# Kernel tuning notes

Measured on AMD Instinct MI355X. Metric: run time of the kernel, lower is better.

The kernel has to match this reference:

```python
import jax, jax.numpy as jnp
import numpy as np

ENC_H = 128
DEC_H = 256
DEC_STEPS = 10


def _gru_cell(x, h, Wih, Whh, bih, bhh):
    # PyTorch GRU cell, gate order (r, z, n)
    gi = x @ Wih.T + bih          # (B, 3H)
    gh = h @ Whh.T + bhh          # (B, 3H)
    H = h.shape[-1]
    ir, iz, inn = gi[:, :H], gi[:, H:2 * H], gi[:, 2 * H:]
    hr, hz, hn = gh[:, :H], gh[:, H:2 * H], gh[:, 2 * H:]
    r = jax.nn.sigmoid(ir + hr)
    z = jax.nn.sigmoid(iz + hz)
    n = jnp.tanh(inn + r * hn)
    return (1.0 - z) * n + z * h


def setup_inputs() -> dict:
    key = jax.random.key(0)
    ks = jax.random.split(key, 12)
    B, S = 4096, 128
    s = 0.1
    return {
        "x": jax.random.normal(ks[0], (B, S, 5), jnp.float32),
        "y": jax.random.normal(ks[1], (B, S, 1), jnp.float32),
        "enc_Wih": jax.random.normal(ks[2], (3 * ENC_H, 5), jnp.float32) * s,
        "enc_Whh": jax.random.normal(ks[3], (3 * ENC_H, ENC_H), jnp.float32) * s,
        "enc_bih": jax.random.normal(ks[4], (3 * ENC_H,), jnp.float32) * s,
        "enc_bhh": jax.random.normal(ks[5], (3 * ENC_H,), jnp.float32) * s,
        "dec_Wih": jax.random.normal(ks[6], (3 * DEC_H, ENC_H + 1), jnp.float32) * s,
        "dec_Whh": jax.random.normal(ks[7], (3 * DEC_H, DEC_H), jnp.float32) * s,
        "dec_bih": jax.random.normal(ks[8], (3 * DEC_H,), jnp.float32) * s,
        "dec_bhh": jax.random.normal(ks[9], (3 * DEC_H,), jnp.float32) * s,
        "lin_W": jax.random.normal(ks[10], (4, DEC_H), jnp.float32) * s,
        "lin_b": jax.random.normal(ks[11], (4,), jnp.float32) * s,
    }


def reference(x, y, enc_Wih, enc_Whh, enc_bih, enc_bhh,
              dec_Wih, dec_Whh, dec_bih, dec_bhh, lin_W, lin_b):
    B, S, _ = x.shape
    xs = jnp.transpose(x, (1, 0, 2))   # (S, B, 5)
    ys = jnp.transpose(y, (1, 0, 2))   # (S, B, 1)

    # Encoder: only the final hidden state (contex) is consumed downstream.
    h0 = jnp.zeros((B, ENC_H), x.dtype)

    def enc_step(h, xt):
        return _gru_cell(xt, h, enc_Wih, enc_Whh, enc_bih, enc_bhh), None

    contex, _ = jax.lax.scan(enc_step, h0, xs)   # (B, 128)

    # Decoder: initial hidden is ones (torch.ones_like(shape)), 10 steps.
    hdec0 = jnp.ones((B, DEC_H), x.dtype)

    def dec_step(h, yt):
        xt = jnp.concatenate([contex, yt], axis=-1)   # (B, 129)
        h2 = _gru_cell(xt, h, dec_Wih, dec_Whh, dec_bih, dec_bhh)
        out = h2 @ lin_W.T + lin_b                    # (B, 4)
        return h2, out

    _, outs = jax.lax.scan(dec_step, hdec0, ys[:DEC_STEPS])  # (10, B, 4)

    # res starts as ones; only first 10 rows written.
    res = jnp.ones((S, B, 4), x.dtype).at[:DEC_STEPS].set(outs)
    return jnp.transpose(res, (1, 0, 2))   # (B, S, 4)
```

## Files before the change

### kernel.cpp

```cpp
#include <hip/hip_runtime.h>

#define B_SZ 4096
#define S_SZ 128
#define XD 5
#define EH 128
#define DH 256
#define DSTEPS 10

typedef short v8s __attribute__((ext_vector_type(8)));
typedef float v4f __attribute__((ext_vector_type(4)));

__device__ __forceinline__ float bf2f(unsigned short u) {
    union { unsigned int i; float f; } v; v.i = ((unsigned int)u) << 16; return v.f;
}
__device__ __forceinline__ unsigned short f2bf(float f) {
    union { float f; unsigned int i; } v; v.f = f;
    unsigned int x = v.i;
    return (unsigned short)((x + 0x7FFFu + ((x >> 16) & 1u)) >> 16);
}
__device__ __forceinline__ float fexp2(float x) { return __builtin_amdgcn_exp2f(x); }
__device__ __forceinline__ float frcp(float x) { return __builtin_amdgcn_rcpf(x); }
__device__ __forceinline__ float sigmoidf_(float x) {
    return frcp(1.f + fexp2(-1.44269504088896f * x));
}
__device__ __forceinline__ float tanhf_(float x) {
    float e = fexp2(2.88539008177793f * x);
    return 1.f - 2.f * frcp(e + 1.f);
}

__global__ __launch_bounds__(512) void enc_kernel(
    const float* __restrict__ x,
    const float* __restrict__ Wih32,
    const float* __restrict__ Whh32,
    const float* __restrict__ bih,
    const float* __restrict__ bhh,
    const float* __restrict__ dWih,
    const float* __restrict__ dWhh,
    unsigned short* __restrict__ wihp,
    unsigned short* __restrict__ dWhh_bf,
    unsigned short* __restrict__ ctex)
{
    __shared__ unsigned short xs[S_SZ][16][8];
    __shared__ unsigned short hb[2][16][136];
    __shared__ unsigned short zpad[8];

    const int tid = threadIdx.x;
    const int bid = blockIdx.x;
    const int wv = tid >> 6;
    const int lane = tid & 63;
    const int n = lane & 15;
    const int kg = lane >> 4;
    const int r0 = bid * 16;

    for (int i = bid * 512 + tid; i < 768 * 256; i += 131072)
        dWhh_bf[i] = f2bf(dWhh[i]);
    for (int i = bid * 512 + tid; i < 768 * 136; i += 131072) {
        int col = i / 136, k = i - col * 136;
        wihp[i] = (k < 129) ? f2bf(dWih[col * 129 + k]) : (unsigned short)0;
    }

    for (int i = tid; i < 2 * 16 * 136; i += 512) ((unsigned short*)hb)[i] = 0;
    if (tid < 8) zpad[tid] = 0;
    for (int i = tid; i < 16 * S_SZ * 8; i += 512) {
        int m = i >> 10;
        int rem = i & 1023;
        int t = rem >> 3;
        int j = rem & 7;
        unsigned short v = 0;
        if (j < XD) v = f2bf(x[(size_t)(r0 + m) * (S_SZ * XD) + t * XD + j]);
        xs[t][m][j] = v;
    }

    const int colw = wv * 16 + n;
    v8s fw[3][4];
    v8s fx[3];
    #pragma unroll
    for (int g = 0; g < 3; ++g) {
        int gcol = g * EH + colw;
        #pragma unroll
        for (int kt = 0; kt < 4; ++kt) {
            const float* p = &Whh32[(size_t)gcol * EH + kt * 32 + kg * 8];
            float4 lo = *(const float4*)p;
            float4 hi = *(const float4*)(p + 4);
            v8s f;
            f[0] = (short)f2bf(lo.x); f[1] = (short)f2bf(lo.y);
            f[2] = (short)f2bf(lo.z); f[3] = (short)f2bf(lo.w);
            f[4] = (short)f2bf(hi.x); f[5] = (short)f2bf(hi.y);
            f[6] = (short)f2bf(hi.z); f[7] = (short)f2bf(hi.w);
            fw[g][kt] = f;
        }
        v8s t = {0, 0, 0, 0, 0, 0, 0, 0};
        if (kg == 0) {
            const float* p = &Wih32[gcol * XD];
            #pragma unroll
            for (int j = 0; j < XD; ++j) t[j] = (short)f2bf(p[j]);
        }
        fx[g] = t;
    }
    const float b_r  = bih[colw]          + bhh[colw];
    const float b_z  = bih[EH + colw]     + bhh[EH + colw];
    const float bi_n = bih[2 * EH + colw];
    const float bh_n = bhh[2 * EH + colw];

    float hst[4] = {0.f, 0.f, 0.f, 0.f};
    __syncthreads();

    #pragma unroll 2
    for (int t = 0; t < S_SZ; ++t) {
        const int p = t & 1;
        v8s a[4];
        #pragma unroll
        for (int kt = 0; kt < 4; ++kt)
            a[kt] = *(const v8s*)&hb[p][n][kt * 32 + kg * 8];
        const unsigned short* xsrc = (kg == 0) ? &xs[t][n][0] : &zpad[0];
        v8s ax = *(const v8s*)xsrc;

        v4f accr  = {b_r, b_r, b_r, b_r};
        v4f accz  = {b_z, b_z, b_z, b_z};
        v4f acchn = {bh_n, bh_n, bh_n, bh_n};
        v4f accin = {bi_n, bi_n, bi_n, bi_n};
        #pragma unroll
        for (int kt = 0; kt < 4; ++kt) {
            accr  = __builtin_amdgcn_mfma_f32_16x16x32_bf16(a[kt], fw[0][kt], accr, 0, 0, 0);
            accz  = __builtin_amdgcn_mfma_f32_16x16x32_bf16(a[kt], fw[1][kt], accz, 0, 0, 0);
            acchn = __builtin_amdgcn_mfma_f32_16x16x32_bf16(a[kt], fw[2][kt], acchn, 0, 0, 0);
        }
        accr  = __builtin_amdgcn_mfma_f32_16x16x32_bf16(ax, fx[0], accr, 0, 0, 0);
        accz  = __builtin_amdgcn_mfma_f32_16x16x32_bf16(ax, fx[1], accz, 0, 0, 0);
        accin = __builtin_amdgcn_mfma_f32_16x16x32_bf16(ax, fx[2], accin, 0, 0, 0);

        #pragma unroll
        for (int e = 0; e < 4; ++e) {
            float r = sigmoidf_(accr[e]);
            float z = sigmoidf_(accz[e]);
            float nn = tanhf_(accin[e] + r * acchn[e]);
            float h = (1.f - z) * nn + z * hst[e];
            hst[e] = h;
            hb[1 - p][kg * 4 + e][colw] = f2bf(h);
        }
        __syncthreads();
    }
    #pragma unroll
    for (int e = 0; e < 4; ++e)
        ctex[(size_t)(r0 + kg * 4 + e) * EH + colw] = f2bf(hst[e]);
}

__global__ __launch_bounds__(1024)
__attribute__((amdgpu_waves_per_eu(4, 4)))
void dec_all_kernel(
    const unsigned short* __restrict__ dWhh_bf,
    const unsigned short* __restrict__ wihp,
    const float* __restrict__ dbih,
    const float* __restrict__ dbhh,
    const float* __restrict__ y,
    const unsigned short* __restrict__ ctex,
    const float* __restrict__ linW,
    const float* __restrict__ linb,
    float* __restrict__ out)
{
    __shared__ unsigned short hshf[32 * 16 * 8];
    __shared__ unsigned short wshnf[32 * 256 * 8];
    __shared__ unsigned short lwf[32 * 16 * 8];

    const int tid = threadIdx.x;
    const int w = tid >> 6;
    const int lane = tid & 63;
    const int n = lane & 15;
    const int kg = lane >> 4;
    const int rb = blockIdx.x * 16;
    const int hcol = w * 16 + n;

    for (int i = tid; i < 8192; i += 1024) {
        int wcol = i >> 5, kc = i & 31;
        uint4 v = *(const uint4*)&dWhh_bf[(size_t)(512 + wcol) * 256 + kc * 8];
        *(uint4*)&wshnf[(kc * 256 + wcol) * 8] = v;
    }
    if (tid < 512) {
        int col = tid >> 5, kc = tid & 31;
        unsigned short v8[8];
        #pragma unroll
        for (int j = 0; j < 8; ++j)
            v8[j] = (col < 4) ? f2bf(linW[col * 256 + kc * 8 + j]) : (unsigned short)0;
        *(uint4*)&lwf[(kc * 16 + col) * 8] = *(uint4*)v8;
    }
    for (int i = tid; i < 32 * 16 * 8; i += 1024) hshf[i] = 0x3F80;

    v8s fB[2][8];
    #pragma unroll
    for (int g = 0; g < 2; ++g)
        #pragma unroll
        for (int kt = 0; kt < 8; ++kt)
            fB[g][kt] = *(const v8s*)&dWhh_bf[(size_t)(g * 256 + hcol) * 256 + kt * 32 + kg * 8];

    const float bR0 = dbih[hcol] + dbhh[hcol];
    const float bZ0 = dbih[DH + hcol] + dbhh[DH + hcol];
    const float bN0 = dbih[2 * DH + hcol];
    const float bN  = dbhh[2 * DH + hcol];
    const float wy0 = bf2f(wihp[(size_t)(0 * DH + hcol) * 136 + 128]);
    const float wy1 = bf2f(wihp[(size_t)(1 * DH + hcol) * 136 + 128]);
    const float wy2 = bf2f(wihp[(size_t)(2 * DH + hcol) * 136 + 128]);

    v4f gvr = {bR0, bR0, bR0, bR0};
    v4f gvz = {bZ0, bZ0, bZ0, bZ0};
    v4f gvn = {bN0, bN0, bN0, bN0};
    #pragma unroll
    for (int kt = 0; kt < 4; ++kt) {
        v8s a  = *(const v8s*)&ctex[(size_t)(rb + n) * EH + kt * 32 + kg * 8];
        v8s b0 = *(const v8s*)&wihp[(size_t)(0 * DH + hcol) * 136 + kt * 32 + kg * 8];
        v8s b1 = *(const v8s*)&wihp[(size_t)(1 * DH + hcol) * 136 + kt * 32 + kg * 8];
        v8s b2 = *(const v8s*)&wihp[(size_t)(2 * DH + hcol) * 136 + kt * 32 + kg * 8];
        gvr = __builtin_amdgcn_mfma_f32_16x16x32_bf16(a, b0, gvr, 0, 0, 0);
        gvz = __builtin_amdgcn_mfma_f32_16x16x32_bf16(a, b1, gvz, 0, 0, 0);
        gvn = __builtin_amdgcn_mfma_f32_16x16x32_bf16(a, b2, gvn, 0, 0, 0);
    }

    const float lb = linb[n & 3];
    const int wfrag = ((w >> 1) * 4 + ((2 * w + (n >> 3)) & 3)) * 128 + (n & 7);

    float hprev[4] = {1.f, 1.f, 1.f, 1.f};
    __syncthreads();

    for (int t = 0; t < DSTEPS; ++t) {
        float yv[4];
        #pragma unroll
        for (int e = 0; e < 4; ++e)
            yv[e] = y[(size_t)(rb + kg * 4 + e) * S_SZ + t];

        v4f accr = {0.f, 0.f, 0.f, 0.f};
        v4f accz = {0.f, 0.f, 0.f, 0.f};
        v4f accn = {bN, bN, bN, bN};
        #pragma unroll
        for (int kt = 0; kt < 8; ++kt) {
            v8s a   = *(const v8s*)&hshf[((kt * 4 + kg) * 16 + n) * 8];
            v8s bn_ = *(const v8s*)&wshnf[((kt * 4 + kg) * 256 + hcol) * 8];
            accr = __builtin_amdgcn_mfma_f32_16x16x32_bf16(a, fB[0][kt], accr, 0, 0, 0);
            accz = __builtin_amdgcn_mfma_f32_16x16x32_bf16(a, fB[1][kt], accz, 0, 0, 0);
            accn = __builtin_amdgcn_mfma_f32_16x16x32_bf16(a, bn_,      accn, 0, 0, 0);
        }
        __syncthreads();

        #pragma unroll
        for (int e = 0; e < 4; ++e) {
            float r  = sigmoidf_(gvr[e] + yv[e] * wy0 + accr[e]);
            float z  = sigmoidf_(gvz[e] + yv[e] * wy1 + accz[e]);
            float nn = tanhf_(gvn[e] + yv[e] * wy2 + r * accn[e]);
            float h  = nn + z * (hprev[e] - nn);
            hprev[e] = h;
            hshf[wfrag + (kg * 4 + e) * 8] = f2bf(h);
        }
        __syncthreads();

        if (w == 0) {
            v4f o4 = {0.f, 0.f, 0.f, 0.f};
            #pragma unroll
            for (int kt = 0; kt < 8; ++kt) {
                v8s a = *(const v8s*)&hshf[((kt * 4 + kg) * 16 + n) * 8];
                v8s b = *(const v8s*)&lwf[((kt * 4 + kg) * 16 + n) * 8];
                o4 = __builtin_amdgcn_mfma_f32_16x16x32_bf16(a, b, o4, 0, 0, 0);
            }
            if (n < 4) {
                #pragma unroll
                for (int e = 0; e < 4; ++e)
                    out[(size_t)(rb + kg * 4 + e) * (S_SZ * 4) + t * 4 + n] = o4[e] + lb;
            }
        }
    }

    for (int j = tid; j < 16 * 512; j += 1024) {
        int row = j >> 9, c = j & 511;
        if (c >= DSTEPS * 4) out[(size_t)(rb + row) * 512 + c] = 1.0f;
    }
}

extern "C" void kernel_launch(void* const* d_in, const int* in_sizes, int n_in,
                              void* d_out, int out_size, void* d_ws, size_t ws_size,
                              hipStream_t stream)
{
    const float* x    = (const float*)d_in[0];
    const float* y    = (const float*)d_in[1];
    const float* eWih = (const float*)d_in[2];
    const float* eWhh = (const float*)d_in[3];
    const float* ebih = (const float*)d_in[4];
    const float* ebhh = (const float*)d_in[5];
    const float* dWih = (const float*)d_in[6];
    const float* dWhh = (const float*)d_in[7];
    const float* dbih = (const float*)d_in[8];
    const float* dbhh = (const float*)d_in[9];
    const float* linW = (const float*)d_in[10];
    const float* linb = (const float*)d_in[11];
    float* out = (float*)d_out;

    char* ws = (char*)d_ws;
    unsigned short* wihp    = (unsigned short*)(ws);
    unsigned short* dWhh_bf = (unsigned short*)(ws + 208896);
    unsigned short* ctex    = (unsigned short*)(ws + 602112);

    enc_kernel<<<256, 512, 0, stream>>>(x, eWih, eWhh, ebih, ebhh,
                                        dWih, dWhh, wihp, dWhh_bf, ctex);
    dec_all_kernel<<<256, 1024, 0, stream>>>(dWhh_bf, wihp, dbih, dbhh, y,
                                             ctex, linW, linb, out);
}
```

Measured before the change: 220.3 us.

## Halve decoder block to 8 waves, each computing two column groups

The decoder kernel now runs 512 threads per block instead of 1024. Each wave covers 32 hidden columns (two 16-column groups), so one A-fragment load from the shared hidden state serves two sets of MFMAs. The shared n-gate weight buffer gets a padded row stride of 264 to cut LDS bank conflicts. Register pressure roughly doubles per thread (more weight fragments and accumulators), and there are fewer waves to hide latency, while the encoder is untouched.

```diff
diff --git a/kernel.cpp b/kernel.cpp
--- a/kernel.cpp
+++ b/kernel.cpp
@@ -145,8 +145,8 @@
         ctex[(size_t)(r0 + kg * 4 + e) * EH + colw] = f2bf(hst[e]);
 }
 
-__global__ __launch_bounds__(1024)
-__attribute__((amdgpu_waves_per_eu(4, 4)))
+__global__ __launch_bounds__(512)
+__attribute__((amdgpu_waves_per_eu(2, 2)))
 void dec_all_kernel(
     const unsigned short* __restrict__ dWhh_bf,
     const unsigned short* __restrict__ wihp,
@@ -158,66 +158,78 @@
     const float* __restrict__ linb,
     float* __restrict__ out)
 {
+    __shared__ unsigned short wshn[32 * 264 * 8];
     __shared__ unsigned short hshf[32 * 16 * 8];
-    __shared__ unsigned short wshnf[32 * 256 * 8];
     __shared__ unsigned short lwf[32 * 16 * 8];
 
-    const int tid = threadIdx.x;
-    const int w = tid >> 6;
+    const int tid  = threadIdx.x;
+    const int w    = tid >> 6;
     const int lane = tid & 63;
-    const int n = lane & 15;
-    const int kg = lane >> 4;
-    const int rb = blockIdx.x * 16;
-    const int hcol = w * 16 + n;
-
-    for (int i = tid; i < 8192; i += 1024) {
-        int wcol = i >> 5, kc = i & 31;
-        uint4 v = *(const uint4*)&dWhh_bf[(size_t)(512 + wcol) * 256 + kc * 8];
-        *(uint4*)&wshnf[(kc * 256 + wcol) * 8] = v;
-    }
-    if (tid < 512) {
-        int col = tid >> 5, kc = tid & 31;
+    const int n    = lane & 15;
+    const int kg   = lane >> 4;
+    const int rb   = blockIdx.x * 16;
+    const int cbase = w * 32;
+
+    for (int i = tid; i < 256 * 32; i += 512) {
+        int col = i >> 5, kgrp = i & 31;
+        uint4 v = *(const uint4*)&dWhh_bf[(size_t)(512 + col) * 256 + kgrp * 8];
+        *(uint4*)&wshn[(kgrp * 264 + col) * 8] = v;
+    }
+    {
+        int col = tid >> 5, kgrp = tid & 31;
         unsigned short v8[8];
         #pragma unroll
         for (int j = 0; j < 8; ++j)
-            v8[j] = (col < 4) ? f2bf(linW[col * 256 + kc * 8 + j]) : (unsigned short)0;
-        *(uint4*)&lwf[(kc * 16 + col) * 8] = *(uint4*)v8;
-    }
-    for (int i = tid; i < 32 * 16 * 8; i += 1024) hshf[i] = 0x3F80;
-
-    v8s fB[2][8];
+            v8[j] = (col < 4) ? f2bf(linW[col * 256 + kgrp * 8 + j]) : (unsigned short)0;
+        *(uint4*)&lwf[(kgrp * 16 + col) * 8] = *(uint4*)v8;
+    }
+    for (int i = tid; i < 32 * 16 * 8; i += 512) hshf[i] = 0x3F80;
+
+    v8s fB[2][2][8];
     #pragma unroll
     for (int g = 0; g < 2; ++g)
         #pragma unroll
-        for (int kt = 0; kt < 8; ++kt)
-            fB[g][kt] = *(const v8s*)&dWhh_bf[(size_t)(g * 256 + hcol) * 256 + kt * 32 + kg * 8];
-
-    const float bR0 = dbih[hcol] + dbhh[hcol];
-    const float bZ0 = dbih[DH + hcol] + dbhh[DH + hcol];
-    const float bN0 = dbih[2 * DH + hcol];
-    const float bN  = dbhh[2 * DH + hcol];
-    const float wy0 = bf2f(wihp[(size_t)(0 * DH + hcol) * 136 + 128]);
-    const float wy1 = bf2f(wihp[(size_t)(1 * DH + hcol) * 136 + 128]);
-    const float wy2 = bf2f(wihp[(size_t)(2 * DH + hcol) * 136 + 128]);
-
-    v4f gvr = {bR0, bR0, bR0, bR0};
-    v4f gvz = {bZ0, bZ0, bZ0, bZ0};
-    v4f gvn = {bN0, bN0, bN0, bN0};
+        for (int cg = 0; cg < 2; ++cg)
+            #pragma unroll
+            for (int kt = 0; kt < 8; ++kt)
+                fB[g][cg][kt] = *(const v8s*)
+                    &dWhh_bf[(size_t)(g * DH + cbase + cg * 16 + n) * DH + kt * 32 + kg * 8];
+
+    v4f gi[3][2];
+    float wy[3][2], bNh[2];
+    #pragma unroll
+    for (int g = 0; g < 3; ++g)
+        #pragma unroll
+        for (int cg = 0; cg < 2; ++cg) {
+            int gcol = g * DH + cbase + cg * 16 + n;
+            float bb = dbih[gcol] + ((g < 2) ? dbhh[gcol] : 0.f);
+            gi[g][cg] = (v4f){bb, bb, bb, bb};
+            wy[g][cg] = bf2f(wihp[(size_t)gcol * 136 + 128]);
+        }
+    #pragma unroll
+    for (int cg = 0; cg < 2; ++cg)
+        bNh[cg] = dbhh[2 * DH + cbase + cg * 16 + n];
+
     #pragma unroll
     for (int kt = 0; kt < 4; ++kt) {
-        v8s a  = *(const v8s*)&ctex[(size_t)(rb + n) * EH + kt * 32 + kg * 8];
-        v8s b0 = *(const v8s*)&wihp[(size_t)(0 * DH + hcol) * 136 + kt * 32 + kg * 8];
-        v8s b1 = *(const v8s*)&wihp[(size_t)(1 * DH + hcol) * 136 + kt * 32 + kg * 8];
-        v8s b2 = *(const v8s*)&wihp[(size_t)(2 * DH + hcol) * 136 + kt * 32 + kg * 8];
-        gvr = __builtin_amdgcn_mfma_f32_16x16x32_bf16(a, b0, gvr, 0, 0, 0);
-        gvz = __builtin_amdgcn_mfma_f32_16x16x32_bf16(a, b1, gvz, 0, 0, 0);
-        gvn = __builtin_amdgcn_mfma_f32_16x16x32_bf16(a, b2, gvn, 0, 0, 0);
-    }
-
-    const float lb = linb[n & 3];
-    const int wfrag = ((w >> 1) * 4 + ((2 * w + (n >> 3)) & 3)) * 128 + (n & 7);
-
-    float hprev[4] = {1.f, 1.f, 1.f, 1.f};
+        v8s a = *(const v8s*)&ctex[(size_t)(rb + n) * EH + kt * 32 + kg * 8];
+        #pragma unroll
+        for (int g = 0; g < 3; ++g)
+            #pragma unroll
+            for (int cg = 0; cg < 2; ++cg) {
+                v8s b = *(const v8s*)
+                    &wihp[(size_t)(g * DH + cbase + cg * 16 + n) * 136 + kt * 32 + kg * 8];
+                gi[g][cg] = __builtin_amdgcn_mfma_f32_16x16x32_bf16(a, b, gi[g][cg], 0, 0, 0);
+            }
+    }
+
+    const float lb = (n < 4) ? linb[n] : 0.f;
+    float hprev[2][4];
+    #pragma unroll
+    for (int cg = 0; cg < 2; ++cg)
+        #pragma unroll
+        for (int e = 0; e < 4; ++e) hprev[cg][e] = 1.0f;
+
     __syncthreads();
 
     for (int t = 0; t < DSTEPS; ++t) {
@@ -226,27 +238,38 @@
         for (int e = 0; e < 4; ++e)
             yv[e] = y[(size_t)(rb + kg * 4 + e) * S_SZ + t];
 
-        v4f accr = {0.f, 0.f, 0.f, 0.f};
-        v4f accz = {0.f, 0.f, 0.f, 0.f};
-        v4f accn = {bN, bN, bN, bN};
+        v4f ar[2], az[2], an[2];
+        #pragma unroll
+        for (int cg = 0; cg < 2; ++cg) {
+            ar[cg] = (v4f){0.f, 0.f, 0.f, 0.f};
+            az[cg] = (v4f){0.f, 0.f, 0.f, 0.f};
+            an[cg] = (v4f){bNh[cg], bNh[cg], bNh[cg], bNh[cg]};
+        }
         #pragma unroll
         for (int kt = 0; kt < 8; ++kt) {
-            v8s a   = *(const v8s*)&hshf[((kt * 4 + kg) * 16 + n) * 8];
-            v8s bn_ = *(const v8s*)&wshnf[((kt * 4 + kg) * 256 + hcol) * 8];
-            accr = __builtin_amdgcn_mfma_f32_16x16x32_bf16(a, fB[0][kt], accr, 0, 0, 0);
-            accz = __builtin_amdgcn_mfma_f32_16x16x32_bf16(a, fB[1][kt], accz, 0, 0, 0);
-            accn = __builtin_amdgcn_mfma_f32_16x16x32_bf16(a, bn_,      accn, 0, 0, 0);
+            v8s a = *(const v8s*)&hshf[((kt * 4 + kg) * 16 + n) * 8];
+            #pragma unroll
+            for (int cg = 0; cg < 2; ++cg) {
+                v8s bn_ = *(const v8s*)&wshn[((kt * 4 + kg) * 264 + cbase + cg * 16 + n) * 8];
+                ar[cg] = __builtin_amdgcn_mfma_f32_16x16x32_bf16(a, fB[0][cg][kt], ar[cg], 0, 0, 0);
+                az[cg] = __builtin_amdgcn_mfma_f32_16x16x32_bf16(a, fB[1][cg][kt], az[cg], 0, 0, 0);
+                an[cg] = __builtin_amdgcn_mfma_f32_16x16x32_bf16(a, bn_,           an[cg], 0, 0, 0);
+            }
         }
         __syncthreads();
 
         #pragma unroll
-        for (int e = 0; e < 4; ++e) {
-            float r  = sigmoidf_(gvr[e] + yv[e] * wy0 + accr[e]);
-            float z  = sigmoidf_(gvz[e] + yv[e] * wy1 + accz[e]);
-            float nn = tanhf_(gvn[e] + yv[e] * wy2 + r * accn[e]);
-            float h  = nn + z * (hprev[e] - nn);
-            hprev[e] = h;
-            hshf[wfrag + (kg * 4 + e) * 8] = f2bf(h);
+        for (int cg = 0; cg < 2; ++cg) {
+            const int chi = 4 * w + 2 * cg + (n >> 3);
+            #pragma unroll
+            for (int e = 0; e < 4; ++e) {
+                float r  = sigmoidf_(gi[0][cg][e] + yv[e] * wy[0][cg] + ar[cg][e]);
+                float z  = sigmoidf_(gi[1][cg][e] + yv[e] * wy[1][cg] + az[cg][e]);
+                float nn = tanhf_(gi[2][cg][e] + yv[e] * wy[2][cg] + r * an[cg][e]);
+                float h  = nn + z * (hprev[cg][e] - nn);
+                hprev[cg][e] = h;
+                hshf[(chi * 16 + kg * 4 + e) * 8 + (n & 7)] = f2bf(h);
+            }
         }
         __syncthreads();
 
@@ -266,7 +289,7 @@
         }
     }
 
-    for (int j = tid; j < 16 * 512; j += 1024) {
+    for (int j = tid; j < 16 * 512; j += 512) {
         int row = j >> 9, c = j & 511;
         if (c >= DSTEPS * 4) out[(size_t)(rb + row) * 512 + c] = 1.0f;
     }
@@ -297,6 +320,6 @@
 
     enc_kernel<<<256, 512, 0, stream>>>(x, eWih, eWhh, ebih, ebhh,
                                         dWih, dWhh, wihp, dWhh_bf, ctex);
-    dec_all_kernel<<<256, 1024, 0, stream>>>(dWhh_bf, wihp, dbih, dbhh, y,
-                                             ctex, linW, linb, out);
-}
+    dec_all_kernel<<<256, 512, 0, stream>>>(dWhh_bf, wihp, dbih, dbhh, y,
+                                            ctex, linW, linb, out);
+}
```

Measured after the change: 217.4 us. No clear change (-1.3%).
